# Optimization experiments

Measured on AMD Instinct MI355X. Metric: run time of the kernel, lower is better.

Reference implementation:

```python
import jax, jax.numpy as jnp
import numpy as np

B, N = 2, 4096
IN_CH, OUT_CH = 64, 64
L_MAX, NR = 3, 4
KERNEL_RADIUS = 0.5
PATCH = 64  # hardcoded in torch topk(-dist, 64)


def setup_inputs() -> dict:
    key = jax.random.key(0)
    k1, k2, k3 = jax.random.split(key, 3)
    xyz = jax.random.normal(k1, (B, N, 3), dtype=jnp.float32)
    signal = jax.random.normal(k2, (B, N, IN_CH), dtype=jnp.float32)
    # xavier_uniform on (out, in, nr, l_max+1): receptive = nr*(l_max+1)
    recept = NR * (L_MAX + 1)
    bound = float(np.sqrt(6.0 / (IN_CH * recept + OUT_CH * recept)))
    weight = jax.random.uniform(k3, (OUT_CH, IN_CH, NR, L_MAX + 1), dtype=jnp.float32,
                                minval=-bound, maxval=bound)
    biases = jnp.zeros((OUT_CH,), dtype=jnp.float32)
    return {"xyz": xyz, "signal": signal, "weight": weight, "biases": biases}


def _sph(X):
    # X: [B,N,P,3] l2-normalized patch directions -> [B,N,P,(L_MAX+1)^2]
    x, y, z = X[..., 0], X[..., 1], X[..., 2]
    x2, y2, z2 = x * x, y * y, z * z
    Ys = []
    Ys.append(jnp.full_like(x, 0.5 * np.sqrt(1.0 / np.pi)))           # Y00
    s3 = np.sqrt(3.0 / np.pi) / 2.0
    Ys += [s3 * y, s3 * z, -s3 * x]                                    # l=1
    s15h = np.sqrt(15.0 / np.pi) / 2.0
    s15q = np.sqrt(15.0 / np.pi) / 4.0
    s5q = np.sqrt(5.0 / np.pi) / 4.0
    Ys += [s15h * x * y, s15h * y * z, s5q * (2.0 * z2 - x2 - y2),
           -s15h * z * x, s15q * (x2 - y2)]                            # l=2
    c33 = np.sqrt(35.0 / (2.0 * np.pi)) / 4.0
    c32 = np.sqrt(105.0 / np.pi) / 2.0
    c31 = np.sqrt(21.0 / (2.0 * np.pi)) / 4.0
    c30 = np.sqrt(7.0 / np.pi) / 4.0
    c32b = np.sqrt(105.0 / np.pi) / 4.0
    Ys += [c33 * (3.0 * x2 * y - y * y2),
           c32 * x * y * z,
           c31 * (4.0 * y * z2 - x2 * y - y * y2),
           c30 * (2.0 * z * z2 - 3.0 * x2 * z - 3.0 * y2 * z),
           -c31 * (4.0 * z2 * x - x * x2 - x * y2),
           c32b * (x2 * z - y2 * z),
           -c33 * (x * x2 - 3.0 * x * y2)]                             # l=3
    return jnp.stack(Ys, axis=-1)


def reference(xyz, signal, weight, biases):
    # pairwise squared distances via matmul (costly_cdist)
    r2 = jnp.sum(xyz * xyz, axis=2)                                    # [B,N]
    sqd = r2[:, :, None] - 2.0 * jnp.einsum('bnd,bmd->bnm', xyz, xyz) + r2[:, None, :]
    neg_vals, idx = jax.lax.top_k(-sqd, PATCH)                         # KNN
    sq_patches_dist = -neg_vals                                        # [B,N,P]
    gather = jax.vmap(lambda pts, i: pts[i])                           # per-batch fancy gather
    patches = gather(xyz, idx) - xyz[:, :, None, :]                    # [B,N,P,3]
    # F.normalize(p=2, dim=-1, eps=0.01): x / max(||x||, eps)
    nrm = jnp.linalg.norm(patches, axis=-1, keepdims=True)
    Y = _sph(patches / jnp.maximum(nrm, 0.01))                         # [B,N,P,K2]
    dist = jnp.sqrt(jnp.maximum(sq_patches_dist, 1e-4))                # [B,N,P]
    r_grid = jnp.linspace(0.0, KERNEL_RADIUS, NR, dtype=jnp.float32)   # [NR]
    sigma = KERNEL_RADIUS / (NR - 1)
    rad = jnp.exp(-jnp.square(dist[..., None] - r_grid) / (2.0 * sigma ** 2))  # [B,N,P,NR]
    yk = Y[:, :, :, None, :] * rad[..., None]                          # [B,N,P,NR,K2]
    y_w = jnp.sum(yk[:, :, :, 0, 0], axis=2)[:, :, None, None, None]   # [B,N,1,1,1]
    conv_kernel = yk / (y_w + 1e-6)
    sig_patches = gather(signal, idx)                                  # [B,N,P,C]
    y = jnp.einsum('bvprn,bvpc->bvcrn', conv_kernel, sig_patches)
    y = y * y
    bands = [jnp.sum(y[..., l * l:(l + 1) * (l + 1)], axis=-1) for l in range(L_MAX + 1)]
    y = jnp.stack(bands, axis=-1)                                      # [B,N,C,NR,L+1]
    y = jnp.sqrt(jnp.maximum(y, 1e-4))
    out = jnp.einsum('ijrn,bvjrn->bvi', weight, y) + biases
    return out
```

## Files before the change

kernel.cpp:

```cpp
#include <hip/hip_runtime.h>
#include <hip/hip_bf16.h>
#include <math.h>

#define NB 2
#define NPTS 4096
#define CH 64
#define PATCH 64

typedef __attribute__((ext_vector_type(8))) short s16x8;
typedef __attribute__((ext_vector_type(4))) short s16x4;
typedef __attribute__((ext_vector_type(4))) float f32x4;
typedef __attribute__((ext_vector_type(4))) unsigned u32x4;

static __device__ __forceinline__ short f2bf(float f) {
    union { __hip_bfloat16 h; short s; } u;
    u.h = __float2bfloat16(f);
    return u.s;
}

__global__ __launch_bounds__(256) void prep_kernel(const float* __restrict__ W,
                                                   short* __restrict__ Wfrag,
                                                   const float* __restrict__ xyz,
                                                   float4* __restrict__ xyz4) {
    const int bid = blockIdx.x;
    const int tid = threadIdx.x;
    if (bid < 32) {
        const int gid = bid * 256 + tid;
        const int mt = gid >> 11;
        const int st = (gid >> 6) & 31;
        const int l  = gid & 63;
        const int i  = mt * 16 + (l & 15);
        const int k0 = st * 32 + (l >> 4) * 8;
        const f32x4 a = *(const f32x4*)&W[i * 1024 + k0];
        const f32x4 c = *(const f32x4*)&W[i * 1024 + k0 + 4];
        s16x8 v;
        v[0] = f2bf(a[0]); v[1] = f2bf(a[1]); v[2] = f2bf(a[2]); v[3] = f2bf(a[3]);
        v[4] = f2bf(c[0]); v[5] = f2bf(c[1]); v[6] = f2bf(c[2]); v[7] = f2bf(c[3]);
        *(s16x8*)&Wfrag[gid * 8] = v;
    } else {
        const int idx = (bid - 32) * 256 + tid;
        float4 v;
        v.x = xyz[idx * 3 + 0];
        v.y = xyz[idx * 3 + 1];
        v.z = xyz[idx * 3 + 2];
        v.w = 0.0f;
        xyz4[idx] = v;
    }
}

__global__ __launch_bounds__(256, 6) void knn_kernel(const float4* __restrict__ xyz4,
                                                     int* __restrict__ knn_idx) {
    const int pt   = blockIdx.x;
    const int b    = pt >> 12;
    const int q    = pt & (NPTS - 1);
    const int tid  = threadIdx.x;
    const int wv   = tid >> 6;
    const int lane = tid & 63;

    __shared__ __align__(16) unsigned hist[4096];
    __shared__ __align__(16) unsigned short sbin[4096];
    __shared__ unsigned wsum[4];
    __shared__ unsigned sh_H;
    __shared__ int sh_need;
    __shared__ int cnt_less, cnt_tie;

    const float4* xb = xyz4 + (size_t)b * NPTS;
    const float4 qp = xb[q];

#pragma unroll
    for (int u = 0; u < 4; ++u)
        ((u32x4*)hist)[u * 256 + tid] = (u32x4){0u, 0u, 0u, 0u};
    if (tid == 0) { cnt_less = 0; cnt_tie = 0; }
    __syncthreads();

#pragma unroll 4
    for (int i = 0; i < 16; ++i) {
        const int m = i * 256 + tid;
        const float4 p = xb[m];
        const float dx = p.x - qp.x;
        const float dy = p.y - qp.y;
        const float dz = p.z - qp.z;
        const float sq = fmaf(dx, dx, fmaf(dy, dy, dz * dz));
        const unsigned hk = __float_as_uint(sq) >> 19;
        sbin[i * 256 + tid] = (unsigned short)hk;
        atomicAdd(&hist[hk], 1u);
    }
    __syncthreads();

    unsigned tsum = 0;
#pragma unroll
    for (int u = 0; u < 4; ++u) {
        const u32x4 h4 = ((const u32x4*)hist)[tid * 4 + u];
        tsum += h4[0] + h4[1] + h4[2] + h4[3];
    }
    unsigned run = tsum;
#pragma unroll
    for (int off = 1; off < 64; off <<= 1) {
        const unsigned v = __shfl_up(run, off);
        if (lane >= off) run += v;
    }
    if (lane == 63) wsum[wv] = run;
    __syncthreads();
    unsigned wbase = 0;
    for (int w2 = 0; w2 < wv; ++w2) wbase += wsum[w2];
    const unsigned incl = wbase + run;
    const unsigned excl = incl - tsum;
    if ((int)excl < PATCH && PATCH <= (int)incl) {
        int nrem = PATCH - (int)excl;
        for (int u = 0; u < 16; ++u) {
            const unsigned cb = hist[tid * 16 + u];
            if (nrem <= (int)cb) { sh_H = (unsigned)(tid * 16 + u); sh_need = nrem; break; }
            nrem -= (int)cb;
        }
    }
    __syncthreads();

    const unsigned H = sh_H;
    const int need  = sh_need;
    const int nless = PATCH - need;
    int* optr = knn_idx + (size_t)pt * PATCH;
    unsigned* ckey = hist;
    unsigned* cidx = hist + 2048;

#pragma unroll 4
    for (int i = 0; i < 16; ++i) {
        const int m = i * 256 + tid;
        const unsigned hk = sbin[i * 256 + tid];
        if (hk < H) {
            const int pos = atomicAdd(&cnt_less, 1);
            optr[pos] = m;
        } else if (hk == H) {
            const int pos = atomicAdd(&cnt_tie, 1);
            if (pos < 2048) {
                const float4 p = xb[m];
                const float dx = p.x - qp.x;
                const float dy = p.y - qp.y;
                const float dz = p.z - qp.z;
                const float sq = fmaf(dx, dx, fmaf(dy, dy, dz * dz));
                ckey[pos] = __float_as_uint(sq);
                cidx[pos] = m;
            }
        }
    }
    __syncthreads();

    const int nc = min(cnt_tie, 2048);
    for (int i = tid; i < nc; i += 256) {
        const unsigned ki = ckey[i];
        int rank = 0;
        for (int j = 0; j < nc; ++j) {
            const unsigned kj = ckey[j];
            rank += (kj < ki || (kj == ki && j < i)) ? 1 : 0;
        }
        if (rank < need) optr[nless + rank] = cidx[i];
    }
}

__global__ __launch_bounds__(256, 4) void conv_kernel(const float4* __restrict__ xyz4,
                                                      const float* __restrict__ signal,
                                                      const short* __restrict__ Wfrag,
                                                      const float* __restrict__ biases,
                                                      const int* __restrict__ knn_idx,
                                                      float* __restrict__ out) {
    const int tid  = threadIdx.x;
    const int wv   = tid >> 6;
    const int lane = tid & 63;
    const int ln15 = lane & 15;
    const int kq   = lane >> 4;

    __shared__ __align__(16) short cks_bf[4096];
    __shared__ __align__(16) short ckF[4096];
    __shared__ __align__(16) short sigF[4096];
    __shared__ __align__(16) short zb[4 * 1032];
    __shared__ int   sIdx[PATCH];
    __shared__ float sh_inv;

    for (int it = 0; it < 4; ++it) {
        const int pt = blockIdx.x * 4 + it;
        const int b  = pt >> 12;
        const int q  = pt & (NPTS - 1);

        if (tid < PATCH) sIdx[tid] = knn_idx[(size_t)pt * PATCH + tid];
        __syncthreads();

        if (wv == 0) {
            const int p   = lane;
            const int idx = sIdx[p];
            const float4 cp = xyz4[(size_t)b * NPTS + q];
            const float4 np = xyz4[(size_t)b * NPTS + idx];
            const float dx = np.x - cp.x;
            const float dy = np.y - cp.y;
            const float dz = np.z - cp.z;
            const float nrm2 = dx * dx + dy * dy + dz * dz;
            const float inv_n = 1.0f / fmaxf(sqrtf(nrm2), 0.01f);
            const float x = dx * inv_n, y = dy * inv_n, z = dz * inv_n;
            const float x2 = x * x, y2 = y * y, zz = z * z;

            float Y[16];
            Y[0] = 0.28209479177387814f;
            const float s3 = 0.4886025119029199f;
            Y[1] = s3 * y;  Y[2] = s3 * z;  Y[3] = -s3 * x;
            const float s15h = 1.0925484305920792f;
            const float s15q = 0.5462742152960396f;
            const float s5q  = 0.31539156525252005f;
            Y[4] = s15h * x * y;
            Y[5] = s15h * y * z;
            Y[6] = s5q * (2.0f * zz - x2 - y2);
            Y[7] = -s15h * z * x;
            Y[8] = s15q * (x2 - y2);
            const float c33  = 0.5900435899266435f;
            const float c32  = 2.8906114426405543f;
            const float c31  = 0.4570457994644658f;
            const float c30  = 0.3731763325901154f;
            const float c32b = 1.4453057213202771f;
            Y[9]  = c33 * (3.0f * x2 * y - y * y2);
            Y[10] = c32 * x * y * z;
            Y[11] = c31 * (4.0f * y * zz - x2 * y - y * y2);
            Y[12] = c30 * (2.0f * z * zz - 3.0f * x2 * z - 3.0f * y2 * z);
            Y[13] = -c31 * (4.0f * zz * x - x * x2 - x * y2);
            Y[14] = c32b * (x2 * z - y2 * z);
            Y[15] = -c33 * (x * x2 - 3.0f * x * y2);

            const float dist = sqrtf(fmaxf(nrm2, 1e-4f));
            const float d1 = dist - 0.16666667f;
            const float d2 = dist - 0.33333334f;
            const float d3 = dist - 0.5f;
            float rad[4];
            rad[0] = expf(-dist * dist * 18.0f);
            rad[1] = expf(-d1 * d1 * 18.0f);
            rad[2] = expf(-d2 * d2 * 18.0f);
            rad[3] = expf(-d3 * d3 * 18.0f);

            const int pm = p & 15;
#pragma unroll
            for (int chunk = 0; chunk < 16; ++chunk) {
                const int r  = chunk >> 2;
                const int kb = (chunk & 3) * 4;
                s16x4 v;
                v[0] = f2bf(Y[kb + 0] * rad[r]);
                v[1] = f2bf(Y[kb + 1] * rad[r]);
                v[2] = f2bf(Y[kb + 2] * rad[r]);
                v[3] = f2bf(Y[kb + 3] * rad[r]);
                *(s16x4*)&cks_bf[p * 64 + ((chunk ^ pm) << 2)] = v;
            }
            float v = 0.28209479177387814f * rad[0];
#pragma unroll
            for (int off = 32; off > 0; off >>= 1) v += __shfl_down(v, off);
            if (p == 0) sh_inv = 1.0f / (v + 1e-6f);
        } else {
            const int r0 = (wv - 1) * 3;
            const int rn = (wv == 3) ? 2 : 3;
            for (int rr = 0; rr < rn; ++rr) {
                const int rd = r0 + rr;
                const int ct = rd >> 1, s = rd & 1;
                const int c  = ct * 16 + ln15;
                const int pb = s * 32 + kq * 8;
                s16x8 sv;
#pragma unroll
                for (int j = 0; j < 8; ++j) {
                    const float f = signal[(size_t)(b * NPTS + sIdx[pb + j]) * CH + c];
                    sv[j] = f2bf(f);
                }
                *(s16x8*)&sigF[(ct * 2 + s) * 512 + lane * 8] = sv;
            }
        }
        __syncthreads();

#pragma unroll
        for (int ff = 0; ff < 2; ++ff) {
            const int f  = wv + ff * 4;
            const int mt = f >> 1, s = f & 1;
            const int rk = mt * 16 + ln15;
            const int rsw = rk >> 2, rlo = rk & 3;
            const int pb = s * 32 + kq * 8;
            s16x8 av;
#pragma unroll
            for (int j = 0; j < 8; ++j) {
                const int p = pb + j;
                av[j] = cks_bf[p * 64 + ((rsw ^ (p & 15)) << 2) + rlo];
            }
            *(s16x8*)&ckF[f * 512 + lane * 8] = av;
        }
        __syncthreads();

        const s16x8 bf0 = *(const s16x8*)&sigF[(wv * 2 + 0) * 512 + lane * 8];
        const s16x8 bf1 = *(const s16x8*)&sigF[(wv * 2 + 1) * 512 + lane * 8];
        f32x4 acc0 = {0.f, 0.f, 0.f, 0.f}, acc1 = acc0, acc2 = acc0, acc3 = acc0;
        {
            s16x8 a;
            a = *(const s16x8*)&ckF[0 * 512 + lane * 8];
            acc0 = __builtin_amdgcn_mfma_f32_16x16x32_bf16(a, bf0, acc0, 0, 0, 0);
            a = *(const s16x8*)&ckF[1 * 512 + lane * 8];
            acc0 = __builtin_amdgcn_mfma_f32_16x16x32_bf16(a, bf1, acc0, 0, 0, 0);
            a = *(const s16x8*)&ckF[2 * 512 + lane * 8];
            acc1 = __builtin_amdgcn_mfma_f32_16x16x32_bf16(a, bf0, acc1, 0, 0, 0);
            a = *(const s16x8*)&ckF[3 * 512 + lane * 8];
            acc1 = __builtin_amdgcn_mfma_f32_16x16x32_bf16(a, bf1, acc1, 0, 0, 0);
            a = *(const s16x8*)&ckF[4 * 512 + lane * 8];
            acc2 = __builtin_amdgcn_mfma_f32_16x16x32_bf16(a, bf0, acc2, 0, 0, 0);
            a = *(const s16x8*)&ckF[5 * 512 + lane * 8];
            acc2 = __builtin_amdgcn_mfma_f32_16x16x32_bf16(a, bf1, acc2, 0, 0, 0);
            a = *(const s16x8*)&ckF[6 * 512 + lane * 8];
            acc3 = __builtin_amdgcn_mfma_f32_16x16x32_bf16(a, bf0, acc3, 0, 0, 0);
            a = *(const s16x8*)&ckF[7 * 512 + lane * 8];
            acc3 = __builtin_amdgcn_mfma_f32_16x16x32_bf16(a, bf1, acc3, 0, 0, 0);
        }

        const float inv = sh_inv;
        const int qq = kq;
        float rb[4][4];
#pragma unroll
        for (int mt = 0; mt < 4; ++mt) {
            f32x4 av = (mt == 0) ? acc0 : (mt == 1) ? acc1 : (mt == 2) ? acc2 : acc3;
            const float y0 = av[0] * inv, y1 = av[1] * inv;
            const float y2 = av[2] * inv, y3 = av[3] * inv;
            const float sA = y0 * y0;
            const float sB = y1 * y1 + y2 * y2 + y3 * y3;
            const float sAll = sA + sB;
            float b0 = (qq == 0) ? sA : 0.0f;
            float b1 = (qq == 0) ? sB : 0.0f;
            float b2 = (qq == 1) ? sAll : ((qq == 2) ? sA : 0.0f);
            float b3 = (qq == 3) ? sAll : ((qq == 2) ? sB : 0.0f);
            b0 += __shfl_xor(b0, 16); b0 += __shfl_xor(b0, 32);
            b1 += __shfl_xor(b1, 16); b1 += __shfl_xor(b1, 32);
            b2 += __shfl_xor(b2, 16); b2 += __shfl_xor(b2, 32);
            b3 += __shfl_xor(b3, 16); b3 += __shfl_xor(b3, 32);
            rb[mt][0] = b0; rb[mt][1] = b1; rb[mt][2] = b2; rb[mt][3] = b3;
        }
        float s0 = rb[0][0], s1 = rb[0][1], s2 = rb[0][2], s3 = rb[0][3];
#pragma unroll
        for (int mt = 1; mt < 4; ++mt) {
            s0 = (qq == mt) ? rb[mt][0] : s0;
            s1 = (qq == mt) ? rb[mt][1] : s1;
            s2 = (qq == mt) ? rb[mt][2] : s2;
            s3 = (qq == mt) ? rb[mt][3] : s3;
        }
        s16x4 zv;
        zv[0] = f2bf(sqrtf(fmaxf(s0, 1e-4f)));
        zv[1] = f2bf(sqrtf(fmaxf(s1, 1e-4f)));
        zv[2] = f2bf(sqrtf(fmaxf(s2, 1e-4f)));
        zv[3] = f2bf(sqrtf(fmaxf(s3, 1e-4f)));
        const int c = wv * 16 + ln15;
        *(s16x4*)&zb[it * 1032 + c * 16 + qq * 4] = zv;
    }
    __syncthreads();

    const int mt5 = wv;
    const int g   = ln15 & 3;
    f32x4 acc5 = {0.f, 0.f, 0.f, 0.f};
#pragma unroll 4
    for (int st = 0; st < 32; ++st) {
        const s16x8 a  = *(const s16x8*)&Wfrag[((mt5 * 32 + st) * 64 + lane) * 8];
        const s16x8 zf = *(const s16x8*)&zb[g * 1032 + st * 32 + kq * 8];
        acc5 = __builtin_amdgcn_mfma_f32_16x16x32_bf16(a, zf, acc5, 0, 0, 0);
    }
    if (ln15 < 4) {
        const int i0 = mt5 * 16 + kq * 4;
        const int orow = (blockIdx.x * 4 + g) * CH;
#pragma unroll
        for (int rg = 0; rg < 4; ++rg)
            out[orow + i0 + rg] = acc5[rg] + biases[i0 + rg];
    }
}

extern "C" void kernel_launch(void* const* d_in, const int* in_sizes, int n_in,
                              void* d_out, int out_size, void* d_ws, size_t ws_size,
                              hipStream_t stream) {
    const float* xyz    = (const float*)d_in[0];
    const float* signal = (const float*)d_in[1];
    const float* weight = (const float*)d_in[2];
    const float* biases = (const float*)d_in[3];
    float* out = (float*)d_out;

    char* ws = (char*)d_ws;
    int*    knn_idx = (int*)ws;
    short*  Wfrag   = (short*)(ws + (size_t)NB * NPTS * PATCH * sizeof(int));
    float4* xyz4    = (float4*)(ws + (size_t)NB * NPTS * PATCH * sizeof(int) + 131072);

    prep_kernel<<<64, 256, 0, stream>>>(weight, Wfrag, xyz, xyz4);
    knn_kernel<<<NB * NPTS, 256, 0, stream>>>(xyz4, knn_idx);
    conv_kernel<<<(NB * NPTS) / 4, 256, 0, stream>>>(xyz4, signal, Wfrag, biases,
                                                     knn_idx, out);
}
```

Measured before the change: 94.98 us.

## Restructure kNN to process four queries per wave with packed 16-bit histograms

After: 118.5 us. +24.8%, slower.

```diff
diff --git a/kernel.cpp b/kernel.cpp
--- a/kernel.cpp
+++ b/kernel.cpp
@@ -6,6 +6,7 @@
 #define NPTS 4096
 #define CH 64
 #define PATCH 64
+#define QPW 4
 
 typedef __attribute__((ext_vector_type(8))) short s16x8;
 typedef __attribute__((ext_vector_type(4))) short s16x4;
@@ -39,120 +40,148 @@
         *(s16x8*)&Wfrag[gid * 8] = v;
     } else {
         const int idx = (bid - 32) * 256 + tid;
+        const float x = xyz[idx * 3 + 0];
+        const float y = xyz[idx * 3 + 1];
+        const float z = xyz[idx * 3 + 2];
         float4 v;
-        v.x = xyz[idx * 3 + 0];
-        v.y = xyz[idx * 3 + 1];
-        v.z = xyz[idx * 3 + 2];
-        v.w = 0.0f;
+        v.x = x; v.y = y; v.z = z;
+        v.w = fmaf(x, x, fmaf(y, y, z * z));
         xyz4[idx] = v;
     }
 }
 
-__global__ __launch_bounds__(256, 6) void knn_kernel(const float4* __restrict__ xyz4,
+__global__ __launch_bounds__(128, 4) void knn_kernel(const float4* __restrict__ xyz4,
                                                      int* __restrict__ knn_idx) {
-    const int pt   = blockIdx.x;
-    const int b    = pt >> 12;
-    const int q    = pt & (NPTS - 1);
     const int tid  = threadIdx.x;
     const int wv   = tid >> 6;
     const int lane = tid & 63;
-
-    __shared__ __align__(16) unsigned hist[4096];
-    __shared__ __align__(16) unsigned short sbin[4096];
-    __shared__ unsigned wsum[4];
-    __shared__ unsigned sh_H;
-    __shared__ int sh_need;
-    __shared__ int cnt_less, cnt_tie;
+    const int wave_id = blockIdx.x * 2 + wv;
+    const int q0 = wave_id * QPW;
+    const int b  = q0 >> 12;
+    const int ql = q0 & (NPTS - 1);
+
+    __shared__ __align__(16) unsigned lds[2 * 2064];
+    unsigned* H01  = lds + wv * 2064;
+    unsigned* H23  = H01 + 1024;
+    unsigned* ctrl = H01 + 2048;
 
     const float4* xb = xyz4 + (size_t)b * NPTS;
-    const float4 qp = xb[q];
-
-#pragma unroll
-    for (int u = 0; u < 4; ++u)
-        ((u32x4*)hist)[u * 256 + tid] = (u32x4){0u, 0u, 0u, 0u};
-    if (tid == 0) { cnt_less = 0; cnt_tie = 0; }
-    __syncthreads();
+
+#pragma unroll
+    for (int i = 0; i < 8; ++i)
+        *(u32x4*)&H01[(i * 64 + lane) * 4] = (u32x4){0u, 0u, 0u, 0u};
+    if (lane < 16) ctrl[lane] = 0u;
+
+    float m2x[QPW], m2y[QPW], m2z[QPW], qw[QPW];
+#pragma unroll
+    for (int i = 0; i < QPW; ++i) {
+        const float4 qp = xb[ql + i];
+        m2x[i] = -2.0f * qp.x; m2y[i] = -2.0f * qp.y; m2z[i] = -2.0f * qp.z;
+        qw[i]  = qp.w;
+    }
+    asm volatile("s_waitcnt lgkmcnt(0)" ::: "memory");
 
 #pragma unroll 4
-    for (int i = 0; i < 16; ++i) {
-        const int m = i * 256 + tid;
+    for (int it = 0; it < 64; ++it) {
+        const int m = it * 64 + lane;
         const float4 p = xb[m];
-        const float dx = p.x - qp.x;
-        const float dy = p.y - qp.y;
-        const float dz = p.z - qp.z;
-        const float sq = fmaf(dx, dx, fmaf(dy, dy, dz * dz));
-        const unsigned hk = __float_as_uint(sq) >> 19;
-        sbin[i * 256 + tid] = (unsigned short)hk;
-        atomicAdd(&hist[hk], 1u);
-    }
-    __syncthreads();
-
-    unsigned tsum = 0;
-#pragma unroll
-    for (int u = 0; u < 4; ++u) {
-        const u32x4 h4 = ((const u32x4*)hist)[tid * 4 + u];
-        tsum += h4[0] + h4[1] + h4[2] + h4[3];
-    }
-    unsigned run = tsum;
-#pragma unroll
-    for (int off = 1; off < 64; off <<= 1) {
-        const unsigned v = __shfl_up(run, off);
-        if (lane >= off) run += v;
-    }
-    if (lane == 63) wsum[wv] = run;
-    __syncthreads();
-    unsigned wbase = 0;
-    for (int w2 = 0; w2 < wv; ++w2) wbase += wsum[w2];
-    const unsigned incl = wbase + run;
-    const unsigned excl = incl - tsum;
-    if ((int)excl < PATCH && PATCH <= (int)incl) {
-        int nrem = PATCH - (int)excl;
-        for (int u = 0; u < 16; ++u) {
-            const unsigned cb = hist[tid * 16 + u];
-            if (nrem <= (int)cb) { sh_H = (unsigned)(tid * 16 + u); sh_need = nrem; break; }
-            nrem -= (int)cb;
-        }
-    }
-    __syncthreads();
-
-    const unsigned H = sh_H;
-    const int need  = sh_need;
-    const int nless = PATCH - need;
-    int* optr = knn_idx + (size_t)pt * PATCH;
-    unsigned* ckey = hist;
-    unsigned* cidx = hist + 2048;
-
-#pragma unroll 4
-    for (int i = 0; i < 16; ++i) {
-        const int m = i * 256 + tid;
-        const unsigned hk = sbin[i * 256 + tid];
-        if (hk < H) {
-            const int pos = atomicAdd(&cnt_less, 1);
-            optr[pos] = m;
-        } else if (hk == H) {
-            const int pos = atomicAdd(&cnt_tie, 1);
-            if (pos < 2048) {
-                const float4 p = xb[m];
-                const float dx = p.x - qp.x;
-                const float dy = p.y - qp.y;
-                const float dz = p.z - qp.z;
-                const float sq = fmaf(dx, dx, fmaf(dy, dy, dz * dz));
-                ckey[pos] = __float_as_uint(sq);
-                cidx[pos] = m;
-            }
-        }
-    }
-    __syncthreads();
-
-    const int nc = min(cnt_tie, 2048);
-    for (int i = tid; i < nc; i += 256) {
-        const unsigned ki = ckey[i];
-        int rank = 0;
-        for (int j = 0; j < nc; ++j) {
-            const unsigned kj = ckey[j];
-            rank += (kj < ki || (kj == ki && j < i)) ? 1 : 0;
-        }
-        if (rank < need) optr[nless + rank] = cidx[i];
+#pragma unroll
+        for (int i = 0; i < QPW; ++i) {
+            float t = fmaf(p.x, m2x[i], p.w);
+            t = fmaf(p.y, m2y[i], t);
+            t = fmaf(p.z, m2z[i], t);
+            t = fmaxf(t + qw[i], 0.0f);
+            const unsigned bin = __float_as_uint(t) >> 21;
+            atomicAdd((i < 2 ? H01 : H23) + bin, (i & 1) ? 0x10000u : 1u);
+        }
+    }
+    asm volatile("s_waitcnt lgkmcnt(0)" ::: "memory");
+
+#pragma unroll
+    for (int i = 0; i < QPW; ++i) {
+        const unsigned* arr = (i < 2) ? H01 : H23;
+        const int sh = (i & 1) * 16;
+        const u32x4 r0 = *(const u32x4*)&arr[lane * 16 + 0];
+        const u32x4 r1 = *(const u32x4*)&arr[lane * 16 + 4];
+        const u32x4 r2 = *(const u32x4*)&arr[lane * 16 + 8];
+        const u32x4 r3 = *(const u32x4*)&arr[lane * 16 + 12];
+        unsigned s = 0;
+#pragma unroll
+        for (int c = 0; c < 4; ++c)
+            s += ((r0[c] >> sh) & 0xFFFFu) + ((r1[c] >> sh) & 0xFFFFu)
+               + ((r2[c] >> sh) & 0xFFFFu) + ((r3[c] >> sh) & 0xFFFFu);
+        unsigned run = s;
+#pragma unroll
+        for (int off = 1; off < 64; off <<= 1) {
+            const unsigned v = __shfl_up(run, off);
+            if (lane >= off) run += v;
+        }
+        const unsigned excl = run - s;
+        if ((int)excl < PATCH && PATCH <= (int)run) {
+            unsigned nrem = PATCH - excl;
+            for (int u = 0; u < 16; ++u) {
+                const unsigned cb = (arr[lane * 16 + u] >> sh) & 0xFFFFu;
+                if (nrem <= cb) { ctrl[8 + i] = (unsigned)(lane * 16 + u);
+                                  ctrl[12 + i] = nrem; break; }
+                nrem -= cb;
+            }
+        }
+    }
+    asm volatile("s_waitcnt lgkmcnt(0)" ::: "memory");
+
+    unsigned Hb[QPW], nd[QPW];
+    int nless[QPW];
+#pragma unroll
+    for (int i = 0; i < QPW; ++i) {
+        Hb[i] = ctrl[8 + i];
+        nd[i] = ctrl[12 + i];
+        nless[i] = PATCH - (int)nd[i];
+    }
+    asm volatile("s_waitcnt lgkmcnt(0)" ::: "memory");
+
+    unsigned* cbuf = H01;
+
+#pragma unroll 2
+    for (int it = 0; it < 64; ++it) {
+        const int m = it * 64 + lane;
+        const float4 p = xb[m];
+#pragma unroll
+        for (int i = 0; i < QPW; ++i) {
+            float t = fmaf(p.x, m2x[i], p.w);
+            t = fmaf(p.y, m2y[i], t);
+            t = fmaf(p.z, m2z[i], t);
+            t = fmaxf(t + qw[i], 0.0f);
+            const unsigned key = __float_as_uint(t);
+            const unsigned bin = key >> 21;
+            if (bin < Hb[i]) {
+                const unsigned pos = atomicAdd(&ctrl[i], 1u);
+                knn_idx[(size_t)(q0 + i) * PATCH + pos] = m;
+            } else if (bin == Hb[i]) {
+                const unsigned pos = atomicAdd(&ctrl[4 + i], 1u);
+                if (pos < 128u) {
+                    cbuf[i * 256 + pos] = key;
+                    cbuf[i * 256 + 128 + pos] = (unsigned)m;
+                }
+            }
+        }
+    }
+    asm volatile("s_waitcnt lgkmcnt(0)" ::: "memory");
+
+    for (int i = 0; i < QPW; ++i) {
+        const int nc = min((int)ctrl[4 + i], 128);
+        const int needi = (int)nd[i];
+        for (int c = lane; c < nc; c += 64) {
+            const unsigned ki = cbuf[i * 256 + c];
+            const unsigned mi = cbuf[i * 256 + 128 + c];
+            int rank = 0;
+            for (int j = 0; j < nc; ++j) {
+                const unsigned kj = cbuf[i * 256 + j];
+                const unsigned mj = cbuf[i * 256 + 128 + j];
+                rank += (kj < ki || (kj == ki && mj < mi)) ? 1 : 0;
+            }
+            if (rank < needi)
+                knn_idx[(size_t)(q0 + i) * PATCH + nless[i] + rank] = (int)mi;
+        }
     }
 }
 
@@ -378,7 +407,7 @@
     float4* xyz4    = (float4*)(ws + (size_t)NB * NPTS * PATCH * sizeof(int) + 131072);
 
     prep_kernel<<<64, 256, 0, stream>>>(weight, Wfrag, xyz, xyz4);
-    knn_kernel<<<NB * NPTS, 256, 0, stream>>>(xyz4, knn_idx);
+    knn_kernel<<<(NB * NPTS) / (2 * QPW), 128, 0, stream>>>(xyz4, knn_idx);
     conv_kernel<<<(NB * NPTS) / 4, 256, 0, stream>>>(xyz4, signal, Wfrag, biases,
                                                      knn_idx, out);
 }
```
